# Performance work log

Measured on AMD Instinct MI355X. Metric: run time of the kernel, lower is better.

## Reference

```python
import jax, jax.numpy as jnp
import numpy as np

# --- constants mirroring init_kwargs ---
DIM = 1024
N_HEADS = 16
N_KV_HEADS = 4
HEAD_DIM = DIM // N_HEADS          # 64
REP = N_HEADS // N_KV_HEADS        # 4
ROPE_THETA = 10000.0
WINDOW = 512
N_GLOBAL = 64
EPS = 1e-6


def setup_inputs() -> dict:
    key = jax.random.key(0)
    ks = jax.random.split(key, 7)
    B, L = 2, 2048
    x = jax.random.normal(ks[0], (B, L, DIM), dtype=jnp.float32)
    s = 0.02
    wq = jax.random.normal(ks[1], (DIM, N_HEADS * HEAD_DIM), dtype=jnp.float32) * s
    wk = jax.random.normal(ks[2], (DIM, N_KV_HEADS * HEAD_DIM), dtype=jnp.float32) * s
    wv = jax.random.normal(ks[3], (DIM, N_KV_HEADS * HEAD_DIM), dtype=jnp.float32) * s
    wo = jax.random.normal(ks[4], (N_HEADS * HEAD_DIM, DIM), dtype=jnp.float32) * s
    gq = jnp.ones((HEAD_DIM,), dtype=jnp.float32) + 0.01 * jax.random.normal(ks[5], (HEAD_DIM,), dtype=jnp.float32)
    gk = jnp.ones((HEAD_DIM,), dtype=jnp.float32) + 0.01 * jax.random.normal(ks[6], (HEAD_DIM,), dtype=jnp.float32)
    return {"x": x, "wq": wq, "wk": wk, "wv": wv, "wo": wo, "gq": gq, "gk": gk}


def _rmsnorm(t, g):
    # QKNorm: RMS norm over head_dim with learnable per-dim scale
    return t * jax.lax.rsqrt(jnp.mean(t * t, axis=-1, keepdims=True) + EPS) * g


def _rope(t, cos, sin):
    # t: [B,H,L,hd]; complex RoPE over consecutive pairs (2i, 2i+1)
    t1 = t[..., 0::2]
    t2 = t[..., 1::2]
    o1 = t1 * cos - t2 * sin
    o2 = t1 * sin + t2 * cos
    return jnp.stack([o1, o2], axis=-1).reshape(t.shape)


def reference(x, wq, wk, wv, wo, gq, gk):
    B, L, D = x.shape
    q = (x @ wq).reshape(B, L, N_HEADS, HEAD_DIM)
    k = (x @ wk).reshape(B, L, N_KV_HEADS, HEAD_DIM)
    v = (x @ wv).reshape(B, L, N_KV_HEADS, HEAD_DIM)
    q = _rmsnorm(q, gq)
    k = _rmsnorm(k, gk)
    q = q.transpose(0, 2, 1, 3)  # [B,H,L,hd]
    k = k.transpose(0, 2, 1, 3)
    v = v.transpose(0, 2, 1, 3)

    # RoPE frequencies (start_pos = 0)
    inv_freq = 1.0 / (ROPE_THETA ** (jnp.arange(0, HEAD_DIM, 2, dtype=jnp.float32) / HEAD_DIM))
    ang = jnp.arange(L, dtype=jnp.float32)[:, None] * inv_freq[None, :]  # [L, hd/2]
    cos, sin = jnp.cos(ang), jnp.sin(ang)
    q = _rope(q, cos, sin)
    k = _rope(k, cos, sin)

    # GQA: repeat kv heads (repeat_interleave on head dim)
    k = jnp.repeat(k, REP, axis=1)
    v = jnp.repeat(v, REP, axis=1)

    scores = jnp.einsum("bhqd,bhkd->bhqk", q, k) / np.sqrt(HEAD_DIM).astype(np.float32)

    # sliding-window + global-token causal mask
    half = WINDOW // 2
    i = jnp.arange(L)[:, None]
    j = jnp.arange(L)[None, :]
    m = (j <= i) & ((j >= i - half) | (j < N_GLOBAL))  # [L,L] bool
    scores = jnp.where(m[None, None], scores, -jnp.inf)

    attn = jax.nn.softmax(scores.astype(jnp.float32), axis=-1).astype(scores.dtype)
    out = jnp.einsum("bhqk,bhkd->bhqd", attn, v)
    out = out.transpose(0, 2, 1, 3).reshape(B, L, N_HEADS * HEAD_DIM)
    return out @ wo
```

## Files before the change

### kernel.cpp

```cpp
#include <hip/hip_runtime.h>
#include <hip/hip_bf16.h>

typedef __bf16 bf16x8 __attribute__((ext_vector_type(8)));
typedef __bf16 bf16x4 __attribute__((ext_vector_type(4)));
typedef float  f32x4  __attribute__((ext_vector_type(4)));
typedef short  s16x4  __attribute__((ext_vector_type(4)));

__device__ __forceinline__ __bf16 to_bf16(float f) {
    __hip_bfloat16 h = __float2bfloat16(f);
    return *reinterpret_cast<__bf16*>(&h);
}

__device__ __forceinline__ f32x4 mfma32(bf16x8 a, bf16x8 b, f32x4 c) {
    return __builtin_amdgcn_mfma_f32_16x16x32_bf16(a, b, c, 0, 0, 0);
}
__device__ __forceinline__ f32x4 mfma16(bf16x4 a, bf16x4 b, f32x4 c) {
#if __has_builtin(__builtin_amdgcn_mfma_f32_16x16x16_bf16)
    return __builtin_amdgcn_mfma_f32_16x16x16_bf16(a, b, c, 0, 0, 0);
#else
    return __builtin_amdgcn_mfma_f32_16x16x16bf16_1k(
        __builtin_bit_cast(s16x4, a), __builtin_bit_cast(s16x4, b), c, 0, 0, 0);
#endif
}

__device__ __forceinline__ void gload_lds16(const __bf16* g, __bf16* l) {
    __builtin_amdgcn_global_load_lds(
        (const __attribute__((address_space(1))) void*)g,
        (__attribute__((address_space(3))) void*)l, 16, 0, 0);
}


__global__ __launch_bounds__(256) void prep_k(const float* __restrict__ wq,
                                              const float* __restrict__ wk,
                                              const float* __restrict__ wv,
                                              const float* __restrict__ wo,
                                              const float* __restrict__ x,
                                              __bf16* __restrict__ WqkvT,
                                              __bf16* __restrict__ WoT,
                                              __bf16* __restrict__ xb,
                                              float2* __restrict__ rope_tab) {
    int b = blockIdx.x, tid = threadIdx.x;
    if (b >= 4608) {
        int idx = (b - 4608) * 256 + tid;
        int pos = idx >> 5, f = idx & 31;
        float ex = (float)(2 * f) * (1.0f / 64.0f);
        float invf = expf(-ex * 9.210340371976184f);
        float ang = (float)pos * invf;
        rope_tab[idx] = make_float2(cosf(ang), sinf(ang));
        return;
    }
    if (b >= 2560) {
        int i = ((b - 2560) * 256 + tid) * 8;
        f32x4 a = *(const f32x4*)(x + i);
        f32x4 c = *(const f32x4*)(x + i + 4);
        bf16x8 h;
        h[0] = to_bf16(a.x); h[1] = to_bf16(a.y); h[2] = to_bf16(a.z); h[3] = to_bf16(a.w);
        h[4] = to_bf16(c.x); h[5] = to_bf16(c.y); h[6] = to_bf16(c.z); h[7] = to_bf16(c.w);
        *(bf16x8*)(xb + i) = h;
        return;
    }
    __shared__ float tile[32][33];
    const float* src; __bf16* dst; int N, idx;
    if (b < 1024)      { src = wq; dst = WqkvT;                        N = 1024; idx = b; }
    else if (b < 1280) { src = wk; dst = WqkvT + (size_t)1024 * 1024;  N = 256;  idx = b - 1024; }
    else if (b < 1536) { src = wv; dst = WqkvT + (size_t)1280 * 1024;  N = 256;  idx = b - 1280; }
    else               { src = wo; dst = WoT;                          N = 1024; idx = b - 1536; }
    int k0 = (idx & 31) * 32, n0 = (idx >> 5) * 32;
    int tx = tid & 31, ty = tid >> 5;
#pragma unroll
    for (int r = 0; r < 4; ++r) {
        int kk = ty + r * 8;
        tile[kk][tx] = src[(size_t)(k0 + kk) * N + n0 + tx];
    }
    __syncthreads();
#pragma unroll
    for (int r = 0; r < 4; ++r) {
        int nn = ty + r * 8;
        dst[(size_t)(n0 + nn) * 1024 + k0 + tx] = to_bf16(tile[tx][nn]);
    }
}

#define GEMM_CORE128(A, BT, K)                                                  \
    __shared__ __bf16 smem[32768];                                              \
    int tid = threadIdx.x;                                                      \
    int m0 = blockIdx.x * 128, n0 = blockIdx.y * 128;                           \
    int wid = tid >> 6, lane = tid & 63;                                        \
    int wm = (wid & 1) * 64, wn = (wid >> 1) * 32;                              \
    int lm = lane & 15, qd = lane >> 4;                                         \
    int srow = tid >> 2, sc4 = tid & 3;                                         \
    f32x4 acc[4][2] = {};                                                       \
    int nt = (K) / 64;                                                          \
    auto STAGE = [&](int bsel, int t) {                                         \
        __bf16* base = smem + bsel * 16384;                                     \
        _Pragma("unroll")                                                       \
        for (int kh = 0; kh < 2; ++kh)                                          \
            gload_lds16((A) + (size_t)(m0 + srow) * (K) + t * 64 + kh * 32 + sc4 * 8, \
                        base + kh * 4096 + wid * 512);                          \
        _Pragma("unroll")                                                       \
        for (int kh = 0; kh < 2; ++kh)                                          \
            gload_lds16((BT) + (size_t)(n0 + srow) * (K) + t * 64 + kh * 32 + sc4 * 8, \
                        base + 8192 + kh * 4096 + wid * 512);                   \
    };                                                                          \
    STAGE(0, 0);                                                                \
    for (int t = 0; t < nt; ++t) {                                              \
        if (t + 1 < nt) {                                                       \
            STAGE((t + 1) & 1, t + 1);                                          \
            asm volatile("s_waitcnt vmcnt(4)" ::: "memory");                    \
        } else {                                                                \
            asm volatile("s_waitcnt vmcnt(0)" ::: "memory");                    \
        }                                                                       \
        __builtin_amdgcn_s_barrier();                                           \
        __builtin_amdgcn_sched_barrier(0);                                      \
        const __bf16* cA = smem + (t & 1) * 16384;                              \
        const __bf16* cB = cA + 8192;                                           \
        _Pragma("unroll")                                                       \
        for (int kh = 0; kh < 2; ++kh) {                                        \
            bf16x8 af[4], bfr[2];                                               \
            _Pragma("unroll")                                                   \
            for (int t4 = 0; t4 < 4; ++t4) {                                    \
                int row = wm + t4 * 16 + lm;                                    \
                af[t4] = *(const bf16x8*)&cA[kh * 4096 + row * 32 + qd * 8];    \
            }                                                                   \
            _Pragma("unroll")                                                   \
            for (int j = 0; j < 2; ++j) {                                       \
                int col = wn + j * 16 + lm;                                     \
                bfr[j] = *(const bf16x8*)&cB[kh * 4096 + col * 32 + qd * 8];    \
            }                                                                   \
            _Pragma("unroll")                                                   \
            for (int ti = 0; ti < 4; ++ti)                                      \
                _Pragma("unroll")                                               \
                for (int tj = 0; tj < 2; ++tj)                                  \
                    acc[ti][tj] = mfma32(af[ti], bfr[tj], acc[ti][tj]);         \
        }                                                                       \
        asm volatile("s_waitcnt lgkmcnt(0)" ::: "memory");                      \
        __builtin_amdgcn_s_barrier();                                           \
    }

__global__ __launch_bounds__(512) void gemmqkv_k(const __bf16* __restrict__ A,
                                                 const __bf16* __restrict__ BT,
                                                 const float2* __restrict__ rope_tab,
                                                 const float* __restrict__ gq,
                                                 const float* __restrict__ gk,
                                                 __bf16* __restrict__ Qb,
                                                 __bf16* __restrict__ Kbl,
                                                 __bf16* __restrict__ Vt) {
    __shared__ float ssp[4][128];
    GEMM_CORE128(A, BT, 1024)
    int head0 = n0 >> 6;
    int quad = wid >> 1;
    int chead = wn & 63;

    if (head0 < 20) {
        int head = head0 + (quad >> 1);
        bool isq = head < 16;
        const float* gvec = isq ? gq : gk;
        float gam[2];
#pragma unroll
        for (int tj = 0; tj < 2; ++tj) gam[tj] = gvec[chead + tj * 16 + lm];

#pragma unroll
        for (int ti = 0; ti < 4; ++ti)
#pragma unroll
            for (int r = 0; r < 4; ++r) {
                float sq = acc[ti][0][r] * acc[ti][0][r] + acc[ti][1][r] * acc[ti][1][r];
                sq += __shfl_xor(sq, 1);
                sq += __shfl_xor(sq, 2);
                sq += __shfl_xor(sq, 4);
                sq += __shfl_xor(sq, 8);
                if (lm == 0) ssp[quad][wm + ti * 16 + qd * 4 + r] = sq;
            }
        __syncthreads();

#pragma unroll
        for (int ti = 0; ti < 4; ++ti)
#pragma unroll
            for (int r = 0; r < 4; ++r) {
                int row = wm + ti * 16 + qd * 4 + r;
                int t = m0 + row;
                int pos = t & 2047, bb = t >> 11;
                float ss = ssp[quad][row] + ssp[quad ^ 1][row];
                float scale = rsqrtf(ss * (1.0f / 64.0f) + 1e-6f);
#pragma unroll
                for (int tj = 0; tj < 2; ++tj) {
                    int cw = chead + tj * 16 + lm;
                    float v = acc[ti][tj][r] * scale * gam[tj];
                    float2 cs = rope_tab[pos * 32 + (cw >> 1)];
                    float pv = __shfl_xor(v, 1);
                    float outv = (cw & 1) ? (pv * cs.y + v * cs.x) : (v * cs.x - pv * cs.y);
                    if (isq) {
                        int kvh = head >> 2, h4 = head & 3;
                        size_t off = (((((size_t)bb * 4 + kvh) * 128 + (pos >> 4)) * 4 + h4) * 16
                                      + (pos & 15)) * 64 + cw;
                        Qb[off] = to_bf16(outv * 0.125f);
                    } else {
                        int kvg = head - 16;
                        Kbl[(((size_t)bb * 4 + kvg) * 2048 + pos) * 64 + cw] = to_bf16(outv);
                    }
                }
            }
    } else {
        __bf16* tvh = smem + (quad >> 1) * 8704;
        int bb = m0 >> 11, pos0 = m0 & 2047;
#pragma unroll
        for (int ti = 0; ti < 4; ++ti)
#pragma unroll
            for (int tj = 0; tj < 2; ++tj)
#pragma unroll
                for (int r = 0; r < 4; ++r) {
                    int row = wm + ti * 16 + qd * 4 + r;
                    int cw = chead + tj * 16 + lm;
                    tvh[cw * 136 + row] = to_bf16(acc[ti][tj][r]);
                }
        __syncthreads();
        int hh = tid >> 8, t8 = tid & 255;
        int kvg = head0 + hh - 20;
        size_t gg = (size_t)bb * 4 + kvg;
        const __bf16* tvr = smem + hh * 8704;
#pragma unroll
        for (int p = 0; p < 4; ++p) {
            int d = p * 16 + (t8 >> 4);
            int tok = (t8 & 15) * 8;
            bf16x8 vvv = *(const bf16x8*)&tvr[d * 136 + tok];
            *(bf16x8*)(Vt + (gg * 64 + d) * 2048 + pos0 + tok) = vvv;
        }
    }
}

__global__ __launch_bounds__(512) void gemm_bf16_k(const __bf16* __restrict__ A,
                                                   const __bf16* __restrict__ BT,
                                                   float* __restrict__ C,
                                                   int K, int N) {
    GEMM_CORE128(A, BT, K)
#pragma unroll
    for (int ti = 0; ti < 4; ++ti)
#pragma unroll
        for (int tj = 0; tj < 2; ++tj)
#pragma unroll
            for (int r = 0; r < 4; ++r) {
                int row = m0 + wm + ti * 16 + qd * 4 + r;
                int col = n0 + wn + tj * 16 + lm;
                C[(size_t)row * N + col] = acc[ti][tj][r];
            }
}

__global__ __launch_bounds__(512) void attn_k(const __bf16* __restrict__ Qb,
                                              const __bf16* __restrict__ Kbl,
                                              const __bf16* __restrict__ Vt,
                                              __bf16* __restrict__ aout) {
    __shared__ __bf16 Kt[2][64 * 64];
    __shared__ __bf16 Vl[2][64 * 64];
    int tid = threadIdx.x, wid = tid >> 6, lane = tid & 63;
    int l15 = lane & 15, quad = lane >> 4;
    int qb = blockIdx.x, kvh = blockIdx.y, b = blockIdx.z;
    int qg = wid >> 2;
    int h4 = wid & 3;
    int iw0 = qb * 32;
    int iw = iw0 + qg * 16;
    int g = b * 4 + kvh;
    int h = kvh * 4 + h4;
    int e7 = l15 & 7;

    int qbi = qb * 2 + qg;
    const __bf16* qp = Qb + ((((size_t)g * 128 + qbi) * 4 + h4) * 16 + l15) * 64 + quad * 8;
    bf16x8 qf0 = *(const bf16x8*)qp;
    bf16x8 qf1 = *(const bf16x8*)(qp + 32);

    int ts = (iw0 - 256) >> 6; if (ts < 1) ts = 1;
    int tmaxb = (iw0 + 31) >> 6;
    int n_all = (tmaxb >= ts) ? (tmaxb - ts + 2) : 1;
    int tmaxw = (iw + 15) >> 6;

    const __bf16* Kg = Kbl + (size_t)g * 2048 * 64;
    const __bf16* Vg = Vt + (size_t)g * 64 * 2048;

    int r0 = tid >> 3, c0 = tid & 7;
    int kl = r0 * 64 + ((c0 ^ (r0 & 7)) * 8);

    bf16x8 kr, vr;
    auto stage_load = [&](int tt) {
        kr = *(const bf16x8*)(Kg + (size_t)tt * 64 * 64 + r0 * 64 + c0 * 8);
        vr = *(const bf16x8*)(Vg + (size_t)r0 * 2048 + tt * 64 + c0 * 8);
    };
    auto stage_write = [&](int buf) {
        *(bf16x8*)&Kt[buf][kl] = kr;
        *(bf16x8*)&Vl[buf][kl] = vr;
    };

    stage_load(0);
    stage_write(0);

    f32x4 o[4] = {};
    float mr = -1e30f, lrp = 0.f;
    int iq = iw + l15;

    for (int idx = 0; idx < n_all; ++idx) {
        int tt = (idx == 0) ? 0 : ts + idx - 1;
        if (idx + 1 < n_all) stage_load(ts + idx);
        __syncthreads();
        int buf = idx & 1;

        f32x4 s[4] = {};
#pragma unroll
        for (int nt = 0; nt < 4; ++nt) {
            const __bf16* kp = &Kt[buf][(nt * 16 + l15) * 64];
            bf16x8 k0 = *(const bf16x8*)(kp + ((quad ^ e7) * 8));
            bf16x8 k1 = *(const bf16x8*)(kp + (((quad + 4) ^ e7) * 8));
            s[nt] = mfma32(k0, qf0, s[nt]);
            s[nt] = mfma32(k1, qf1, s[nt]);
        }

        bool need_mask = (tt >= tmaxw) || (tt >= 1 && tt * 64 < iw + 15 - 256);
        if (need_mask) {
#pragma unroll
            for (int nt = 0; nt < 4; ++nt)
#pragma unroll
                for (int r = 0; r < 4; ++r) {
                    int j = tt * 64 + nt * 16 + quad * 4 + r;
                    bool valid = (j <= iq) && ((j >= iq - 256) || (j < 64));
                    s[nt][r] = valid ? s[nt][r] : -1e30f;
                }
        }

        float mx = -1e30f;
#pragma unroll
        for (int nt = 0; nt < 4; ++nt)
#pragma unroll
            for (int r = 0; r < 4; ++r) mx = fmaxf(mx, s[nt][r]);
        mx = fmaxf(mx, __shfl_xor(mx, 16));
        mx = fmaxf(mx, __shfl_xor(mx, 32));
        float mn = fmaxf(mr, mx);
        float alpha = __expf(mr - mn);
        mr = mn;

        float ps = 0.f;
        bf16x4 pb[4];
#pragma unroll
        for (int nt = 0; nt < 4; ++nt)
#pragma unroll
            for (int r = 0; r < 4; ++r) {
                float pv = __expf(s[nt][r] - mn);
                ps += pv;
                pb[nt][r] = to_bf16(pv);
            }
        lrp = lrp * alpha + ps;

#pragma unroll
        for (int dt = 0; dt < 4; ++dt) {
            o[dt] *= alpha;
            const __bf16* vp = &Vl[buf][(dt * 16 + l15) * 64];
#pragma unroll
            for (int nt = 0; nt < 4; ++nt) {
                int c8 = 2 * nt + (quad >> 1);
                bf16x4 va = *(const bf16x4*)(vp + ((c8 ^ e7) * 8) + (quad & 1) * 4);
                o[dt] = mfma16(va, pb[nt], o[dt]);
            }
        }

        if (idx + 1 < n_all) stage_write((idx + 1) & 1);
    }

    lrp += __shfl_xor(lrp, 16);
    lrp += __shfl_xor(lrp, 32);
    float inv = 1.f / lrp;
    __syncthreads();
    __bf16* pr = (__bf16*)Kt + wid * 16 * 64;
#pragma unroll
    for (int dt = 0; dt < 4; ++dt)
#pragma unroll
        for (int r = 0; r < 4; ++r) {
            int e = dt * 16 + quad * 4 + r;
            int c8 = e >> 3;
            pr[l15 * 64 + ((c8 ^ e7) * 8) + (e & 7)] = to_bf16(o[dt][r] * inv);
        }
    bf16x8 o0 = *(const bf16x8*)(pr + l15 * 64 + (((2 * quad) ^ e7) * 8));
    bf16x8 o1 = *(const bf16x8*)(pr + l15 * 64 + (((2 * quad + 1) ^ e7) * 8));
    __bf16* op = aout + ((size_t)b * 2048 + iw + l15) * 1024 + h * 64 + quad * 16;
    *(bf16x8*)op = o0;
    *(bf16x8*)(op + 8) = o1;
}

extern "C" void kernel_launch(void* const* d_in, const int* in_sizes, int n_in,
                              void* d_out, int out_size, void* d_ws, size_t ws_size,
                              hipStream_t stream) {
    const float* x  = (const float*)d_in[0];
    const float* wq = (const float*)d_in[1];
    const float* wk = (const float*)d_in[2];
    const float* wv = (const float*)d_in[3];
    const float* wo = (const float*)d_in[4];
    const float* gq = (const float*)d_in[5];
    const float* gk = (const float*)d_in[6];
    float* out = (float*)d_out;

    char* ws = (char*)d_ws;
    __bf16*  WqkvT = (__bf16*)ws;
    __bf16*  WoT   = (__bf16*)(ws + 3145728);
    __bf16*  xb_ao = (__bf16*)(ws + 5242880);
    __bf16*  Kbl   = (__bf16*)(ws + 13631488);
    __bf16*  Vt    = (__bf16*)(ws + 15728640);
    __bf16*  Qb    = (__bf16*)(ws + 17825792);
    float2*  rtab  = (float2*)(ws + 26214400);

    prep_k<<<4864, dim3(256), 0, stream>>>(wq, wk, wv, wo, x, WqkvT, WoT, xb_ao, rtab);
    gemmqkv_k<<<dim3(32, 12), dim3(512), 0, stream>>>(xb_ao, WqkvT, rtab, gq, gk, Qb, Kbl, Vt);
    attn_k<<<dim3(64, 4, 2), dim3(512), 0, stream>>>(Qb, Kbl, Vt, xb_ao);
    gemm_bf16_k<<<dim3(32, 8), dim3(512), 0, stream>>>(xb_ao, WoT, out, 1024, 1024);
}
```

Measured before the change: 140.0 us.

## Widen attention block to 64 queries with two heads per wave and tile skipping

The attention kernel now handles 64 query rows per block instead of 32, and each wave processes two query heads that share each K/V fragment read from LDS. This halves the grid and the redundant K/V tile staging per query. It also skips whole KV tiles and 16-column subtiles that fall outside the causal and sliding-window mask, and raises wave priority around the MFMA sections. In exchange each wave holds more registers (two output accumulators), which may lower occupancy, and fewer blocks are launched.

After: 145.7 us. 4.1% more time.

```diff
diff --git a/kernel.cpp b/kernel.cpp
--- a/kernel.cpp
+++ b/kernel.cpp
@@ -159,7 +159,7 @@
         for (int tj = 0; tj < 2; ++tj) gam[tj] = gvec[chead + tj * 16 + lm];
 
 #pragma unroll
-        for (int ti = 0; ti < 4; ++ti)
+    for (int ti = 0; ti < 4; ++ti)
 #pragma unroll
             for (int r = 0; r < 4; ++r) {
                 float sq = acc[ti][0][r] * acc[ti][0][r] + acc[ti][1][r] * acc[ti][1][r];
@@ -247,28 +247,32 @@
                                               const __bf16* __restrict__ Kbl,
                                               const __bf16* __restrict__ Vt,
                                               __bf16* __restrict__ aout) {
-    __shared__ __bf16 Kt[2][64 * 64];
-    __shared__ __bf16 Vl[2][64 * 64];
+    __shared__ __bf16 smem[16384];
     int tid = threadIdx.x, wid = tid >> 6, lane = tid & 63;
     int l15 = lane & 15, quad = lane >> 4;
     int qb = blockIdx.x, kvh = blockIdx.y, b = blockIdx.z;
-    int qg = wid >> 2;
-    int h4 = wid & 3;
-    int iw0 = qb * 32;
+    int qg = wid & 3;
+    int hp = wid >> 2;
+    int iw0 = qb * 64;
     int iw = iw0 + qg * 16;
     int g = b * 4 + kvh;
-    int h = kvh * 4 + h4;
     int e7 = l15 & 7;
 
-    int qbi = qb * 2 + qg;
-    const __bf16* qp = Qb + ((((size_t)g * 128 + qbi) * 4 + h4) * 16 + l15) * 64 + quad * 8;
-    bf16x8 qf0 = *(const bf16x8*)qp;
-    bf16x8 qf1 = *(const bf16x8*)(qp + 32);
+    int qbi = qb * 4 + qg;
+    bf16x8 qf[2][2];
+#pragma unroll
+    for (int j = 0; j < 2; ++j) {
+        const __bf16* qp = Qb + ((((size_t)g * 128 + qbi) * 4 + (hp * 2 + j)) * 16 + l15) * 64
+                         + quad * 8;
+        qf[j][0] = *(const bf16x8*)qp;
+        qf[j][1] = *(const bf16x8*)(qp + 32);
+    }
 
     int ts = (iw0 - 256) >> 6; if (ts < 1) ts = 1;
-    int tmaxb = (iw0 + 31) >> 6;
+    int tmaxb = (iw0 + 63) >> 6;
     int n_all = (tmaxb >= ts) ? (tmaxb - ts + 2) : 1;
     int tmaxw = (iw + 15) >> 6;
+    int lowe = iw - 256;
 
     const __bf16* Kg = Kbl + (size_t)g * 2048 * 64;
     const __bf16* Vg = Vt + (size_t)g * 64 * 2048;
@@ -282,15 +286,15 @@
         vr = *(const bf16x8*)(Vg + (size_t)r0 * 2048 + tt * 64 + c0 * 8);
     };
     auto stage_write = [&](int buf) {
-        *(bf16x8*)&Kt[buf][kl] = kr;
-        *(bf16x8*)&Vl[buf][kl] = vr;
+        *(bf16x8*)&smem[buf * 4096 + kl] = kr;
+        *(bf16x8*)&smem[8192 + buf * 4096 + kl] = vr;
     };
 
     stage_load(0);
     stage_write(0);
 
-    f32x4 o[4] = {};
-    float mr = -1e30f, lrp = 0.f;
+    f32x4 o[2][4] = {};
+    float mr[2] = {-1e30f, -1e30f}, lrp[2] = {0.f, 0.f};
     int iq = iw + l15;
 
     for (int idx = 0; idx < n_all; ++idx) {
@@ -299,84 +303,122 @@
         __syncthreads();
         int buf = idx & 1;
 
-        f32x4 s[4] = {};
-#pragma unroll
-        for (int nt = 0; nt < 4; ++nt) {
-            const __bf16* kp = &Kt[buf][(nt * 16 + l15) * 64];
-            bf16x8 k0 = *(const bf16x8*)(kp + ((quad ^ e7) * 8));
-            bf16x8 k1 = *(const bf16x8*)(kp + (((quad + 4) ^ e7) * 8));
-            s[nt] = mfma32(k0, qf0, s[nt]);
-            s[nt] = mfma32(k1, qf1, s[nt]);
+        bool live = (tt == 0) || (tt <= tmaxw && tt * 64 + 63 >= lowe);
+        if (live) {
+            const __bf16* Ktb = &smem[buf * 4096];
+            const __bf16* Vlb = &smem[8192 + buf * 4096];
+
+            bool lv[4];
+#pragma unroll
+            for (int nt = 0; nt < 4; ++nt) {
+                int j0 = tt * 64 + nt * 16;
+                lv[nt] = (j0 <= iw + 15) && (tt == 0 || j0 + 15 >= lowe);
+            }
+
+            f32x4 s0[4], s1[4];
+            __builtin_amdgcn_s_setprio(1);
+#pragma unroll
+            for (int nt = 0; nt < 4; ++nt) {
+                if (!lv[nt]) continue;
+                const __bf16* kp = &Ktb[(nt * 16 + l15) * 64];
+                bf16x8 k0 = *(const bf16x8*)(kp + ((quad ^ e7) * 8));
+                bf16x8 k1 = *(const bf16x8*)(kp + (((quad + 4) ^ e7) * 8));
+                f32x4 z = {};
+                s0[nt] = mfma32(k1, qf[0][1], mfma32(k0, qf[0][0], z));
+                s1[nt] = mfma32(k1, qf[1][1], mfma32(k0, qf[1][0], z));
+            }
+            __builtin_amdgcn_s_setprio(0);
+
+            bool need_mask = (tt == tmaxw) || (tt >= 1 && tt * 64 < iw + 15 - 256)
+                           || (tt == 0 && qb == 0);
+            if (need_mask) {
+#pragma unroll
+                for (int nt = 0; nt < 4; ++nt) {
+                    if (!lv[nt]) continue;
+#pragma unroll
+                    for (int r = 0; r < 4; ++r) {
+                        int j = tt * 64 + nt * 16 + quad * 4 + r;
+                        bool valid = (j <= iq) && ((j >= iq - 256) || (j < 64));
+                        if (!valid) { s0[nt][r] = -1e30f; s1[nt][r] = -1e30f; }
+                    }
+                }
+            }
+
+            float alpha[2];
+            bf16x4 pb[2][4];
+#pragma unroll
+            for (int j = 0; j < 2; ++j) {
+                f32x4* s = j ? s1 : s0;
+                float mx = -1e30f;
+#pragma unroll
+                for (int nt = 0; nt < 4; ++nt) {
+                    if (!lv[nt]) continue;
+#pragma unroll
+                    for (int r = 0; r < 4; ++r) mx = fmaxf(mx, s[nt][r]);
+                }
+                mx = fmaxf(mx, __shfl_xor(mx, 16));
+                mx = fmaxf(mx, __shfl_xor(mx, 32));
+                float mn = fmaxf(mr[j], mx);
+                alpha[j] = __expf(mr[j] - mn);
+                mr[j] = mn;
+                float ps = 0.f;
+#pragma unroll
+                for (int nt = 0; nt < 4; ++nt) {
+                    if (!lv[nt]) continue;
+#pragma unroll
+                    for (int r = 0; r < 4; ++r) {
+                        float pv = __expf(s[nt][r] - mn);
+                        ps += pv;
+                        pb[j][nt][r] = to_bf16(pv);
+                    }
+                }
+                lrp[j] = lrp[j] * alpha[j] + ps;
+            }
+
+            __builtin_amdgcn_s_setprio(1);
+#pragma unroll
+            for (int dt = 0; dt < 4; ++dt) {
+                o[0][dt] *= alpha[0];
+                o[1][dt] *= alpha[1];
+                const __bf16* vp = &Vlb[(dt * 16 + l15) * 64];
+#pragma unroll
+                for (int nt = 0; nt < 4; ++nt) {
+                    if (!lv[nt]) continue;
+                    int c8 = 2 * nt + (quad >> 1);
+                    bf16x4 va = *(const bf16x4*)(vp + ((c8 ^ e7) * 8) + (quad & 1) * 4);
+                    o[0][dt] = mfma16(va, pb[0][nt], o[0][dt]);
+                    o[1][dt] = mfma16(va, pb[1][nt], o[1][dt]);
+                }
+            }
+            __builtin_amdgcn_s_setprio(0);
         }
 
-        bool need_mask = (tt >= tmaxw) || (tt >= 1 && tt * 64 < iw + 15 - 256);
-        if (need_mask) {
-#pragma unroll
-            for (int nt = 0; nt < 4; ++nt)
-#pragma unroll
-                for (int r = 0; r < 4; ++r) {
-                    int j = tt * 64 + nt * 16 + quad * 4 + r;
-                    bool valid = (j <= iq) && ((j >= iq - 256) || (j < 64));
-                    s[nt][r] = valid ? s[nt][r] : -1e30f;
-                }
-        }
-
-        float mx = -1e30f;
-#pragma unroll
-        for (int nt = 0; nt < 4; ++nt)
-#pragma unroll
-            for (int r = 0; r < 4; ++r) mx = fmaxf(mx, s[nt][r]);
-        mx = fmaxf(mx, __shfl_xor(mx, 16));
-        mx = fmaxf(mx, __shfl_xor(mx, 32));
-        float mn = fmaxf(mr, mx);
-        float alpha = __expf(mr - mn);
-        mr = mn;
-
-        float ps = 0.f;
-        bf16x4 pb[4];
-#pragma unroll
-        for (int nt = 0; nt < 4; ++nt)
+        if (idx + 1 < n_all) stage_write((idx + 1) & 1);
+    }
+
+    __syncthreads();
+#pragma unroll
+    for (int j = 0; j < 2; ++j) {
+        float l = lrp[j];
+        l += __shfl_xor(l, 16);
+        l += __shfl_xor(l, 32);
+        float inv = 1.f / l;
+        __bf16* pr = smem + (wid * 2 + j) * 1024;
+#pragma unroll
+        for (int dt = 0; dt < 4; ++dt)
 #pragma unroll
             for (int r = 0; r < 4; ++r) {
-                float pv = __expf(s[nt][r] - mn);
-                ps += pv;
-                pb[nt][r] = to_bf16(pv);
-            }
-        lrp = lrp * alpha + ps;
-
-#pragma unroll
-        for (int dt = 0; dt < 4; ++dt) {
-            o[dt] *= alpha;
-            const __bf16* vp = &Vl[buf][(dt * 16 + l15) * 64];
-#pragma unroll
-            for (int nt = 0; nt < 4; ++nt) {
-                int c8 = 2 * nt + (quad >> 1);
-                bf16x4 va = *(const bf16x4*)(vp + ((c8 ^ e7) * 8) + (quad & 1) * 4);
-                o[dt] = mfma16(va, pb[nt], o[dt]);
-            }
-        }
-
-        if (idx + 1 < n_all) stage_write((idx + 1) & 1);
-    }
-
-    lrp += __shfl_xor(lrp, 16);
-    lrp += __shfl_xor(lrp, 32);
-    float inv = 1.f / lrp;
-    __syncthreads();
-    __bf16* pr = (__bf16*)Kt + wid * 16 * 64;
-#pragma unroll
-    for (int dt = 0; dt < 4; ++dt)
-#pragma unroll
-        for (int r = 0; r < 4; ++r) {
-            int e = dt * 16 + quad * 4 + r;
-            int c8 = e >> 3;
-            pr[l15 * 64 + ((c8 ^ e7) * 8) + (e & 7)] = to_bf16(o[dt][r] * inv);
-        }
-    bf16x8 o0 = *(const bf16x8*)(pr + l15 * 64 + (((2 * quad) ^ e7) * 8));
-    bf16x8 o1 = *(const bf16x8*)(pr + l15 * 64 + (((2 * quad + 1) ^ e7) * 8));
-    __bf16* op = aout + ((size_t)b * 2048 + iw + l15) * 1024 + h * 64 + quad * 16;
-    *(bf16x8*)op = o0;
-    *(bf16x8*)(op + 8) = o1;
+                int e = dt * 16 + quad * 4 + r;
+                int c8 = e >> 3;
+                pr[l15 * 64 + ((c8 ^ e7) * 8) + (e & 7)] = to_bf16(o[j][dt][r] * inv);
+            }
+        bf16x8 o0 = *(const bf16x8*)(pr + l15 * 64 + (((2 * quad) ^ e7) * 8));
+        bf16x8 o1 = *(const bf16x8*)(pr + l15 * 64 + (((2 * quad + 1) ^ e7) * 8));
+        int h = kvh * 4 + hp * 2 + j;
+        __bf16* op = aout + ((size_t)b * 2048 + iw + l15) * 1024 + h * 64 + quad * 16;
+        *(bf16x8*)op = o0;
+        *(bf16x8*)(op + 8) = o1;
+    }
 }
 
 extern "C" void kernel_launch(void* const* d_in, const int* in_sizes, int n_in,
@@ -402,6 +444,6 @@
 
     prep_k<<<4864, dim3(256), 0, stream>>>(wq, wk, wv, wo, x, WqkvT, WoT, xb_ao, rtab);
     gemmqkv_k<<<dim3(32, 12), dim3(512), 0, stream>>>(xb_ao, WqkvT, rtab, gq, gk, Qb, Kbl, Vt);
-    attn_k<<<dim3(64, 4, 2), dim3(512), 0, stream>>>(Qb, Kbl, Vt, xb_ao);
+    attn_k<<<dim3(32, 4, 2), dim3(512), 0, stream>>>(Qb, Kbl, Vt, xb_ao);
     gemm_bf16_k<<<dim3(32, 8), dim3(512), 0, stream>>>(xb_ao, WoT, out, 1024, 1024);
 }
```

## Move Wo transpose into QKV GEMM launch and swizzle GEMM block order

Applied to the files above, without the earlier changes.

The Wo fp32-to-bf16 transpose is moved out of the prep kernel and handled by 128 extra blocks appended to the QKV GEMM grid, so it runs alongside the GEMM tiles instead of lengthening prep. Both GEMM kernels now remap block IDs so that consecutive blocks share B-matrix column tiles, aiming for better L2 reuse. Shared memory becomes dynamic (64KB) so the transpose blocks and GEMM blocks can share one allocation. The extra blocks may add tail imbalance to the GEMM launch.

Measured after the change: 143.7 us. +2.7%, slower.

```diff
diff --git a/kernel.cpp b/kernel.cpp
--- a/kernel.cpp
+++ b/kernel.cpp
@@ -33,15 +33,13 @@
 __global__ __launch_bounds__(256) void prep_k(const float* __restrict__ wq,
                                               const float* __restrict__ wk,
                                               const float* __restrict__ wv,
-                                              const float* __restrict__ wo,
                                               const float* __restrict__ x,
                                               __bf16* __restrict__ WqkvT,
-                                              __bf16* __restrict__ WoT,
                                               __bf16* __restrict__ xb,
                                               float2* __restrict__ rope_tab) {
     int b = blockIdx.x, tid = threadIdx.x;
-    if (b >= 4608) {
-        int idx = (b - 4608) * 256 + tid;
+    if (b >= 3584) {
+        int idx = (b - 3584) * 256 + tid;
         int pos = idx >> 5, f = idx & 31;
         float ex = (float)(2 * f) * (1.0f / 64.0f);
         float invf = expf(-ex * 9.210340371976184f);
@@ -49,8 +47,8 @@
         rope_tab[idx] = make_float2(cosf(ang), sinf(ang));
         return;
     }
-    if (b >= 2560) {
-        int i = ((b - 2560) * 256 + tid) * 8;
+    if (b >= 1536) {
+        int i = ((b - 1536) * 256 + tid) * 8;
         f32x4 a = *(const f32x4*)(x + i);
         f32x4 c = *(const f32x4*)(x + i + 4);
         bf16x8 h;
@@ -63,8 +61,7 @@
     const float* src; __bf16* dst; int N, idx;
     if (b < 1024)      { src = wq; dst = WqkvT;                        N = 1024; idx = b; }
     else if (b < 1280) { src = wk; dst = WqkvT + (size_t)1024 * 1024;  N = 256;  idx = b - 1024; }
-    else if (b < 1536) { src = wv; dst = WqkvT + (size_t)1280 * 1024;  N = 256;  idx = b - 1280; }
-    else               { src = wo; dst = WoT;                          N = 1024; idx = b - 1536; }
+    else               { src = wv; dst = WqkvT + (size_t)1280 * 1024;  N = 256;  idx = b - 1280; }
     int k0 = (idx & 31) * 32, n0 = (idx >> 5) * 32;
     int tx = tid & 31, ty = tid >> 5;
 #pragma unroll
@@ -80,10 +77,10 @@
     }
 }
 
-#define GEMM_CORE128(A, BT, K)                                                  \
-    __shared__ __bf16 smem[32768];                                              \
+#define GEMM_CORE128(A, BT, K, M0, N0)                                          \
+    __bf16* smem = (__bf16*)smem_raw;                                           \
     int tid = threadIdx.x;                                                      \
-    int m0 = blockIdx.x * 128, n0 = blockIdx.y * 128;                           \
+    int m0 = (M0), n0 = (N0);                                                   \
     int wid = tid >> 6, lane = tid & 63;                                        \
     int wm = (wid & 1) * 64, wn = (wid >> 1) * 32;                              \
     int lm = lane & 15, qd = lane >> 4;                                         \
@@ -141,11 +138,41 @@
                                                  const float2* __restrict__ rope_tab,
                                                  const float* __restrict__ gq,
                                                  const float* __restrict__ gk,
+                                                 const float* __restrict__ wo,
                                                  __bf16* __restrict__ Qb,
                                                  __bf16* __restrict__ Kbl,
-                                                 __bf16* __restrict__ Vt) {
+                                                 __bf16* __restrict__ Vt,
+                                                 __bf16* __restrict__ WoT) {
+    extern __shared__ char smem_raw[];
+    if (blockIdx.y >= 12) {
+        float* scr = (float*)smem_raw;
+        int bidT = (blockIdx.y - 12) * 32 + blockIdx.x;
+        int sub = threadIdx.x >> 8, t8 = threadIdx.x & 255;
+        int tx = t8 & 31, ty = t8 >> 5;
+        float* my = scr + sub * 1056;
+#pragma unroll
+        for (int r = 0; r < 4; ++r) {
+            int tile = bidT * 8 + r * 2 + sub;
+            int k0 = (tile & 31) * 32, n0t = (tile >> 5) * 32;
+            __syncthreads();
+#pragma unroll
+            for (int rr = 0; rr < 4; ++rr) {
+                int kk = ty + rr * 8;
+                my[kk * 33 + tx] = wo[(size_t)(k0 + kk) * 1024 + n0t + tx];
+            }
+            __syncthreads();
+#pragma unroll
+            for (int rr = 0; rr < 4; ++rr) {
+                int nn = ty + rr * 8;
+                WoT[(size_t)(n0t + nn) * 1024 + k0 + tx] = to_bf16(my[tx * 33 + nn]);
+            }
+        }
+        return;
+    }
     __shared__ float ssp[4][128];
-    GEMM_CORE128(A, BT, 1024)
+    int gidb = blockIdx.y * 32 + blockIdx.x;
+    int swzb = (gidb & 7) * 48 + (gidb >> 3);
+    GEMM_CORE128(A, BT, 1024, (swzb & 31) * 128, (swzb >> 5) * 128)
     int head0 = n0 >> 6;
     int quad = wid >> 1;
     int chead = wn & 63;
@@ -230,7 +257,10 @@
                                                    const __bf16* __restrict__ BT,
                                                    float* __restrict__ C,
                                                    int K, int N) {
-    GEMM_CORE128(A, BT, K)
+    extern __shared__ char smem_raw[];
+    int gidb = blockIdx.y * 32 + blockIdx.x;
+    int swzb = (gidb & 7) * 32 + (gidb >> 3);
+    GEMM_CORE128(A, BT, K, (swzb & 31) * 128, (swzb >> 5) * 128)
 #pragma unroll
     for (int ti = 0; ti < 4; ++ti)
 #pragma unroll
@@ -400,8 +430,9 @@
     __bf16*  Qb    = (__bf16*)(ws + 17825792);
     float2*  rtab  = (float2*)(ws + 26214400);
 
-    prep_k<<<4864, dim3(256), 0, stream>>>(wq, wk, wv, wo, x, WqkvT, WoT, xb_ao, rtab);
-    gemmqkv_k<<<dim3(32, 12), dim3(512), 0, stream>>>(xb_ao, WqkvT, rtab, gq, gk, Qb, Kbl, Vt);
+    prep_k<<<3840, dim3(256), 0, stream>>>(wq, wk, wv, x, WqkvT, xb_ao, rtab);
+    gemmqkv_k<<<dim3(32, 16), dim3(512), 65536, stream>>>(xb_ao, WqkvT, rtab, gq, gk, wo,
+                                                          Qb, Kbl, Vt, WoT);
     attn_k<<<dim3(64, 4, 2), dim3(512), 0, stream>>>(Qb, Kbl, Vt, xb_ao);
-    gemm_bf16_k<<<dim3(32, 8), dim3(512), 0, stream>>>(xb_ao, WoT, out, 1024, 1024);
-}
+    gemm_bf16_k<<<dim3(32, 8), dim3(512), 65536, stream>>>(xb_ao, WoT, out, 1024, 1024);
+}
```
